# Optimization experiments

Measured on AMD Instinct MI355X. Metric: run time of the kernel, lower is better.

## Reference

```python
import jax, jax.numpy as jnp
import numpy as np

RANGE_DISP = 32
IND_INPUT_VIEW = np.array([1, 9]) - 1  # 0-based indices of the two input views
TOTAL_VIEWS = 9                         # an_sparse + an_novel
FEAT_CH = 64


def conv2d(x, w, b):
    # x: (N, Cin, H, W), w: (Cout, Cin, kh, kw), SAME padding, stride 1
    y = jax.lax.conv_general_dilated(x, w, (1, 1), 'SAME',
                                     dimension_numbers=('NCHW', 'OIHW', 'NCHW'))
    return y + b[None, :, None, None]


def unfold_1xK(x, K):
    # torch.nn.functional.unfold(x, kernel_size=(1, K)) for x: (M, C, H, W)
    # -> (M, C, K, H*(W-K+1)), column index = h*(W-K+1) + w (row-major).
    M, C, H, W = x.shape
    out_w = W - K + 1
    cols = jnp.arange(out_w)[None, :] + jnp.arange(K)[:, None]  # (K, out_w)
    y = x[:, :, :, cols]             # (M, C, H, K, out_w)
    y = y.transpose(0, 1, 3, 2, 4)   # (M, C, K, H, out_w)
    return y.reshape(M, C, K, H * out_w)


def setup_inputs() -> dict:
    key = jax.random.key(0)
    ks = jax.random.split(key, 24)
    b, an_sparse, an_novel, rp = 2, 2, 7, 32
    K = RANGE_DISP
    ps = rp + K - 1  # 63

    def rn(k, shape, s=1.0):
        return jax.random.normal(k, shape, dtype=jnp.float32) * s

    W = 0.05  # weight init scale
    return {
        'lf_sparse':        rn(ks[0], (b, an_sparse, rp, ps)),
        'flow_sparse':      rn(ks[1], (b, an_sparse, rp, ps)),
        'warped_lf_sparse': rn(ks[2], (b, an_sparse, rp, ps)),
        'patch_left':       rn(ks[3], (b, an_novel, rp, rp)),
        'patch_right':      rn(ks[4], (b, an_novel, rp, rp)),
        # FlowRefNet: 3 -> 64 -> 64 -> 64, 3x3 convs, SAME
        'fr_w1': rn(ks[5], (FEAT_CH, 3, 3, 3), W), 'fr_b1': jnp.zeros((FEAT_CH,), jnp.float32),
        'fr_w2': rn(ks[6], (FEAT_CH, FEAT_CH, 3, 3), W), 'fr_b2': jnp.zeros((FEAT_CH,), jnp.float32),
        'fr_w3': rn(ks[7], (FEAT_CH, FEAT_CH, 3, 3), W), 'fr_b3': jnp.zeros((FEAT_CH,), jnp.float32),
        # MlpNet: per-disparity MLP 67 -> 64 -> 64 -> 1 (weight head) + conf head 64 -> 1
        'mlp_w1': rn(ks[8], (67, 64), W), 'mlp_b1': jnp.zeros((64,), jnp.float32),
        'mlp_w2': rn(ks[9], (64, 64), W), 'mlp_b2': jnp.zeros((64,), jnp.float32),
        'mlp_w3': rn(ks[10], (64, 1), W), 'mlp_b3': jnp.zeros((1,), jnp.float32),
        'conf_w': rn(ks[11], (64, 1), W), 'conf_b': jnp.zeros((1,), jnp.float32),
        # ViewRefNet: 3 -> 64 -> 64 -> 1 convs, residual on novel patch
        'vr_w1': rn(ks[12], (FEAT_CH, 3, 3, 3), W), 'vr_b1': jnp.zeros((FEAT_CH,), jnp.float32),
        'vr_w2': rn(ks[13], (FEAT_CH, FEAT_CH, 3, 3), W), 'vr_b2': jnp.zeros((FEAT_CH,), jnp.float32),
        'vr_w3': rn(ks[14], (1, FEAT_CH, 3, 3), W), 'vr_b3': jnp.zeros((1,), jnp.float32),
    }


def reference(lf_sparse, flow_sparse, warped_lf_sparse, patch_left, patch_right,
              fr_w1, fr_b1, fr_w2, fr_b2, fr_w3, fr_b3,
              mlp_w1, mlp_b1, mlp_w2, mlp_b2, mlp_w3, mlp_b3, conf_w, conf_b,
              vr_w1, vr_b1, vr_w2, vr_b2, vr_w3, vr_b3):
    b, an_sparse, rp, ps = lf_sparse.shape
    an_novel = patch_left.shape[1]
    K = RANGE_DISP
    N = rp * rp

    lf = lf_sparse.reshape(b * an_sparse, 1, rp, ps)
    fl = flow_sparse.reshape(b * an_sparse, 1, rp, ps)
    wp = warped_lf_sparse.reshape(b * an_sparse, 1, rp, ps)

    # FlowRefNet: flow-feature extraction
    h = jax.nn.relu(conv2d(jnp.concatenate([fl, lf, wp], axis=1), fr_w1, fr_b1))
    h = jax.nn.relu(conv2d(h, fr_w2, fr_b2))
    feat = jax.nn.relu(conv2d(h, fr_w3, fr_b3))  # (b*as, 64, rp, ps)

    # angular code: input-view index minus novel-view index
    ind_novel = np.delete(np.arange(TOTAL_VIEWS), IND_INPUT_VIEW)
    ang = jnp.asarray(IND_INPUT_VIEW[None, :] - ind_novel[:, None], dtype=lf.dtype)  # (an, as)
    spatial = (jnp.arange(K) - K // 2).astype(lf.dtype)  # (K,)

    # EPI windows via unfold(kernel=(1, K))
    flow_unf = unfold_1xK(fl, K)[:, 0]  # (b*as, K, N)
    feat_unf = unfold_1xK(feat, K)      # (b*as, 64, K, N)

    sh = (b, an_novel, an_sparse)
    f_flow = jnp.broadcast_to(flow_unf.reshape(b, 1, an_sparse, 1, K, N),  sh + (1, K, N))
    f_feat = jnp.broadcast_to(feat_unf.reshape(b, 1, an_sparse, FEAT_CH, K, N), sh + (FEAT_CH, K, N))
    f_spat = jnp.broadcast_to(spatial.reshape(1, 1, 1, 1, K, 1),           sh + (1, K, N))
    f_ang  = jnp.broadcast_to(ang.reshape(1, an_novel, an_sparse, 1, 1, 1), sh + (1, K, N))
    features = jnp.concatenate([f_flow, f_feat, f_spat, f_ang], axis=3)  # (b, an, as, 67, K, N)
    # -> (b*an*as*N, K, 67) matching permute(0,3,2,1).reshape in torch
    features = features.transpose(0, 1, 2, 5, 4, 3).reshape(-1, K, 67)

    # MlpNet: per-disparity weight + per-sample confidence
    h1 = jax.nn.relu(features @ mlp_w1 + mlp_b1)
    h2 = jax.nn.relu(h1 @ mlp_w2 + mlp_b2)          # (M2, K, 64)
    weight = (h2 @ mlp_w3 + mlp_b3)[..., 0]         # (M2, K)
    conf = (h2.mean(axis=1) @ conf_w + conf_b)[..., 0]  # (M2,)

    weight = jax.nn.softmax(weight.reshape(b, an_novel, an_sparse, N, K), axis=-1)
    confs = jax.nn.softmax(conf.reshape(b, an_novel, an_sparse, N), axis=2)

    # disparity-weighted combination over EPI windows
    epi = unfold_1xK(lf, K)[:, 0].reshape(b, an_sparse, K, N)
    nv = jnp.einsum('bskn,bvsnk->bvsn', epi, weight)   # (b, an, as, N)
    novel = (nv * confs).sum(axis=2)                   # (b, an, N)

    # ViewRefNet: residual refinement
    pn = novel.reshape(b * an_novel, 1, rp, rp)
    pl = patch_left.reshape(b * an_novel, 1, rp, rp)
    pr = patch_right.reshape(b * an_novel, 1, rp, rp)
    g = jax.nn.relu(conv2d(jnp.concatenate([pn, pl, pr], axis=1), vr_w1, vr_b1))
    g = jax.nn.relu(conv2d(g, vr_w2, vr_b2))
    res = conv2d(g, vr_w3, vr_b3)
    out = pn + res
    return out.reshape(b, an_novel, rp, rp)
```

## Files before the change

kernel.cpp:

```cpp
#include <hip/hip_runtime.h>

typedef unsigned short u16;
typedef unsigned int u32;
typedef __bf16 bf16x8 __attribute__((ext_vector_type(8)));
typedef float f32x4 __attribute__((ext_vector_type(4)));
typedef u16 u16x8 __attribute__((ext_vector_type(8)));

__device__ __forceinline__ u16 f2bf(float f) {
    __bf16 h = (__bf16)f;
    return __builtin_bit_cast(u16, h);
}
__device__ __forceinline__ float bf2f(u16 u) {
    unsigned int x = ((unsigned int)u) << 16;
    return __builtin_bit_cast(float, x);
}

union FragU { u16x8 u; bf16x8 v; };

constexpr size_t WB2F  = 0;
constexpr size_t WB3F  = 18432;
constexpr size_t WBV2  = 36864;
constexpr size_t W1T   = 55296;
constexpr size_t W2T   = 57344;
constexpr size_t X1    = 59392;
constexpr size_t X2    = 317440;
constexpr size_t FEATBF= 575488;
constexpr size_t NVOFF = 833536;
constexpr size_t CFOFF = 862208;
constexpr size_t NOVEL = 890880;
constexpr size_t Y1    = 905216;
constexpr size_t Y2    = 1363968;

__global__ __launch_bounds__(256) void conv1feat_kernel(
    const float* __restrict__ in0, const float* __restrict__ in1,
    const float* __restrict__ in2,
    const float* __restrict__ wts, const float* __restrict__ bias,
    u16* __restrict__ out,
    const float* __restrict__ frw2, const float* __restrict__ frw3,
    const float* __restrict__ vrw2,
    const float* __restrict__ mw1, const float* __restrict__ mw2,
    u16* __restrict__ wb2, u16* __restrict__ wb3, u16* __restrict__ wbv,
    u16* __restrict__ w1t, u16* __restrict__ w2t)
{
    constexpr int W = 63, NPX = 2016, H = 32;
    const int t = threadIdx.x;
    if (blockIdx.z == 4) {
        const int tid = (blockIdx.y * 8 + blockIdx.x) * 256 + t;
        for (int i = tid; i < 36864; i += 16384) {
            int tap = i >> 12, och = (i >> 6) & 63, cin = i & 63;
            size_t s = (size_t)och * 576 + cin * 9 + tap;
            wb2[i] = f2bf(frw2[s]);
            wb3[i] = f2bf(frw3[s]);
            wbv[i] = f2bf(vrw2[s]);
        }
        for (int i = tid; i < 4096; i += 16384) {
            int col = i >> 6, r = i & 63;
            w1t[i] = f2bf(mw1[(1 + r) * 64 + col]);
            w2t[i] = f2bf(mw2[r * 64 + col]);
        }
        return;
    }
    const int px = blockIdx.y * 256 + t;
    const int m = blockIdx.z;
    const int og = blockIdx.x;
    if (px >= NPX) return;
    const int y = px / W, x = px - y * W;

    float acc[8];
#pragma unroll
    for (int oc = 0; oc < 8; ++oc) acc[oc] = bias[og * 8 + oc];

#pragma unroll
    for (int cin = 0; cin < 3; ++cin) {
        const float* ip = (cin == 0 ? in0 : (cin == 1 ? in1 : in2)) + (size_t)m * NPX;
        float tap[9];
#pragma unroll
        for (int dy = 0; dy < 3; ++dy) {
            int yy = y + dy - 1;
            bool ry = (yy >= 0) && (yy < H);
#pragma unroll
            for (int dx = 0; dx < 3; ++dx) {
                int xx = x + dx - 1;
                tap[dy * 3 + dx] = (ry && xx >= 0 && xx < W) ? ip[yy * W + xx] : 0.f;
            }
        }
#pragma unroll
        for (int oc = 0; oc < 8; ++oc) {
            const float* wr = wts + (size_t)(og * 8 + oc) * 27 + cin * 9;
#pragma unroll
            for (int j = 0; j < 9; ++j) acc[oc] = fmaf(tap[j], wr[j], acc[oc]);
        }
    }
    u16x8 pk;
#pragma unroll
    for (int oc = 0; oc < 8; ++oc) pk[oc] = f2bf(fmaxf(acc[oc], 0.f));
    *(u16x8*)(out + ((size_t)m * NPX + px) * 64 + og * 8) = pk;
}

template<int W, int NPX>
__global__ __launch_bounds__(256) void convmfma_kernel(
    const u16* __restrict__ in, const u16* __restrict__ wbf,
    const float* __restrict__ bias, u16* __restrict__ out)
{
    constexpr int H = 32;
    const int t = threadIdx.x;
    const int base = blockIdx.x * 64;
    const int ochb = blockIdx.y * 32;
    const int m = blockIdx.z;
    const int w = t >> 6, lane = t & 63, q = lane >> 4, l15 = lane & 15;

    const u16* im = in + (size_t)m * NPX * 64;
    const int pxA = base + w * 16 + l15;
    const int yA = pxA / W, xA = pxA - yA * W;
    const bool pxok = (pxA < NPX);

    f32x4 acc[2];
#pragma unroll
    for (int nt = 0; nt < 2; ++nt) acc[nt] = f32x4{0.f, 0.f, 0.f, 0.f};

#pragma unroll
    for (int tap = 0; tap < 9; ++tap) {
        const int dy = tap / 3 - 1, dx = tap % 3 - 1;
        const bool valid = pxok && (yA + dy >= 0) && (yA + dy < H)
                                && (xA + dx >= 0) && (xA + dx < W);
        const u16* ap = im + (size_t)(pxA + dy * W + dx) * 64;
        FragU a0, a1;
        if (valid) {
            a0 = *(const FragU*)(ap + q * 8);
            a1 = *(const FragU*)(ap + 32 + q * 8);
        } else {
#pragma unroll
            for (int jj = 0; jj < 8; ++jj) { a0.u[jj] = 0; a1.u[jj] = 0; }
        }
#pragma unroll
        for (int nt = 0; nt < 2; ++nt) {
            const u16* bp = wbf + tap * 4096 + (ochb + nt * 16 + l15) * 64;
            FragU b0 = *(const FragU*)(bp + q * 8);
            FragU b1 = *(const FragU*)(bp + 32 + q * 8);
            acc[nt] = __builtin_amdgcn_mfma_f32_16x16x32_bf16(a0.v, b0.v, acc[nt], 0, 0, 0);
            acc[nt] = __builtin_amdgcn_mfma_f32_16x16x32_bf16(a1.v, b1.v, acc[nt], 0, 0, 0);
        }
    }

#pragma unroll
    for (int nt = 0; nt < 2; ++nt) {
        const float bb = bias[ochb + nt * 16 + l15];
#pragma unroll
        for (int e = 0; e < 4; ++e) {
            int pxs = base + w * 16 + q * 4 + e;
            if (pxs < NPX)
                out[((size_t)m * NPX + pxs) * 64 + ochb + nt * 16 + l15] =
                    f2bf(fmaxf(acc[nt][e] + bb, 0.f));
        }
    }
}

__global__ __launch_bounds__(256, 2) void mlp_mfma_kernel(
    const float* __restrict__ lf, const float* __restrict__ flow,
    const u16* __restrict__ feat,
    const u16* __restrict__ w1t, const u16* __restrict__ w2t,
    const float* __restrict__ w1, const float* __restrict__ b1,
    const float* __restrict__ b2,
    const float* __restrict__ w3, const float* __restrict__ b3g,
    const float* __restrict__ cw, const float* __restrict__ cbg,
    float* __restrict__ nv_out, float* __restrict__ cf_out)
{
    constexpr int SBS = 72;
    __shared__ __align__(16) float s_vec[7 * 64];
    __shared__ __align__(16) float s_flow[256];
    __shared__ __align__(16) float s_epi[256];
    __shared__ __align__(16) u16 s_base[256 * SBS];

    const int t = threadIdx.x;
    const int blk = blockIdx.x;
    const int bs = blk >> 7;
    const int n0 = (blk & 127) * 8;
    const int b = bs >> 1, s = bs & 1;
    const int w = t >> 6, lane = t & 63, q = lane >> 4, l15 = lane & 15;

    if (t < 64) {
        s_vec[t]       = b1[t];
        s_vec[64 + t]  = b2[t];
        s_vec[128 + t] = w3[t];
        s_vec[192 + t] = cw[t];
        s_vec[256 + t] = w1[t];
        s_vec[320 + t] = w1[65 * 64 + t];
        s_vec[384 + t] = w1[66 * 64 + t];
    }
    {
        int nl = t >> 5, k = t & 31;
        int n = n0 + nl;
        int a = (bs * 32 + (n >> 5)) * 63 + (n & 31) + k;
        s_flow[t] = flow[a];
        s_epi[t]  = lf[a];
    }
    __syncthreads();

    const float b3s = b3g[0];
    const float cbs = cbg[0];

    FragU w1b[2][4];
#pragma unroll
    for (int ks = 0; ks < 2; ++ks)
#pragma unroll
        for (int nt = 0; nt < 4; ++nt)
            w1b[ks][nt] = *(const FragU*)(w1t + (nt * 16 + l15) * 64 + ks * 32 + q * 8);

    float w1r0pl[4], w1r65pl[4], b1pl[4];
#pragma unroll
    for (int nt = 0; nt < 4; ++nt) {
        int j1 = nt * 16 + l15;
        w1r0pl[nt]  = s_vec[256 + j1];
        w1r65pl[nt] = s_vec[320 + j1];
        b1pl[nt]    = s_vec[j1];
    }

#pragma unroll
    for (int mt = 0; mt < 4; ++mt) {
        const int rbase = w * 64 + mt * 16;
        FragU af[2];
        {
            int r = rbase + l15;
            int n = n0 + (r >> 5);
            int pos = (n >> 5) * 63 + (n & 31) + (r & 31);
            const u16* fp = feat + ((size_t)bs * 2016 + pos) * 64;
            af[0] = *(const FragU*)(fp + q * 8);
            af[1] = *(const FragU*)(fp + 32 + q * 8);
        }
// ... 29 lines not shown
        for (int jj = 0; jj < 8; ++jj)
            w66pl[ks][jj] = s_vec[384 + ks * 32 + q * 8 + jj];

    float b2pl[4][4], w3pl[4][4], cwpl[4][4];
#pragma unroll
    for (int mt = 0; mt < 4; ++mt)
#pragma unroll
        for (int e = 0; e < 4; ++e) {
            b2pl[mt][e] = s_vec[64 + mt * 16 + q * 4 + e];
            w3pl[mt][e] = s_vec[128 + mt * 16 + q * 4 + e];
            cwpl[mt][e] = s_vec[192 + mt * 16 + q * 4 + e];
        }
    float epi_pl[4];
#pragma unroll
    for (int nt = 0; nt < 4; ++nt) epi_pl[nt] = s_epi[w * 64 + nt * 16 + l15];

    for (int v = 0; v < 7; ++v) {
        float ang = (s == 0) ? -(float)(v + 1) : (float)(7 - v);
        f32x4 acc[4][4];
#pragma unroll
        for (int nt = 0; nt < 4; ++nt) {
            FragU bfr[2];
#pragma unroll
            for (int ks = 0; ks < 2; ++ks) {
                const u16x8 raw = *(const u16x8*)(s_base + (w * 64 + nt * 16 + l15) * SBS + ks * 32 + q * 8);
#pragma unroll
                for (int jj = 0; jj < 8; ++jj) {
                    float xv = bf2f(raw[jj]);
                    float hv = fmaxf(xv + ang * w66pl[ks][jj], 0.f);
                    bfr[ks].u[jj] = f2bf(hv);
                }
            }
#pragma unroll
            for (int mt = 0; mt < 4; ++mt) {
                f32x4 d = {0.f, 0.f, 0.f, 0.f};
                d = __builtin_amdgcn_mfma_f32_16x16x32_bf16(w2a[mt][0].v, bfr[0].v, d, 0, 0, 0);
                d = __builtin_amdgcn_mfma_f32_16x16x32_bf16(w2a[mt][1].v, bfr[1].v, d, 0, 0, 0);
                acc[mt][nt] = d;
            }
        }
        float wl[4], cfl[4];
#pragma unroll
        for (int nt = 0; nt < 4; ++nt) {
            float wls = 0.f, cfs = 0.f;
#pragma unroll
            for (int mt = 0; mt < 4; ++mt)
#pragma unroll
                for (int e = 0; e < 4; ++e) {
                    float h2 = fmaxf(acc[mt][nt][e] + b2pl[mt][e], 0.f);
                    wls += h2 * w3pl[mt][e];
                    cfs += h2 * cwpl[mt][e];
                }
            wls += __shfl_xor(wls, 16); wls += __shfl_xor(wls, 32);
            cfs += __shfl_xor(cfs, 16); cfs += __shfl_xor(cfs, 32);
            wl[nt]  = wls + b3s;
            cfl[nt] = cfs;
        }
#pragma unroll
        for (int ni = 0; ni < 2; ++ni) {
            float a0 = wl[ni * 2], a1 = wl[ni * 2 + 1];
            float mx = fmaxf(a0, a1);
#pragma unroll
            for (int msk = 1; msk <= 8; msk <<= 1) mx = fmaxf(mx, __shfl_xor(mx, msk));
            float e0 = __expf(a0 - mx), e1 = __expf(a1 - mx);
            float ssum = e0 + e1;
            float nvp = e0 * epi_pl[ni * 2] + e1 * epi_pl[ni * 2 + 1];
            float cfp = cfl[ni * 2] + cfl[ni * 2 + 1];
#pragma unroll
            for (int msk = 1; msk <= 8; msk <<= 1) {
                ssum += __shfl_xor(ssum, msk);
                nvp  += __shfl_xor(nvp, msk);
                cfp  += __shfl_xor(cfp, msk);
            }
            if (lane == 0) {
                int n = n0 + w * 2 + ni;
                size_t idx = ((size_t)(b * 7 + v) * 2 + s) * 1024 + n;
                nv_out[idx] = nvp / ssum;
                cf_out[idx] = cfp * (1.f / 32.f) + cbs;
            }
        }
    }
}

__global__ __launch_bounds__(256) void refconv1_kernel(
    const float* __restrict__ nv, const float* __restrict__ cf,
    const float* __restrict__ pl, const float* __restrict__ pr,
    const float* __restrict__ wts, const float* __restrict__ bias,
    u16* __restrict__ out, float* __restrict__ novel)
{
    __shared__ float pn[10][32];
    const int t = threadIdx.x;
    const int og = blockIdx.x, pt = blockIdx.y, m = blockIdx.z;
    const int y0 = pt * 8;

    for (int i = t; i < 320; i += 256) {
        int ri = i >> 5, col = i & 31;
        int gy = y0 - 1 + ri;
        float vv = 0.f;
        if (gy >= 0 && gy < 32) {
            int n = gy * 32 + col;
            size_t i0 = ((size_t)m * 2) * 1024 + n;
            size_t i1 = i0 + 1024;
            float c0 = cf[i0], c1 = cf[i1];
            float mx = fmaxf(c0, c1);
            float e0 = __expf(c0 - mx), e1 = __expf(c1 - mx);
            vv = (e0 * nv[i0] + e1 * nv[i1]) / (e0 + e1);
        }
        pn[ri][col] = vv;
    }
    __syncthreads();

    const int px = y0 * 32 + t;
    const int y = px >> 5, x = px & 31;
    if (og == 0) novel[(size_t)m * 1024 + px] = pn[y - y0 + 1][x];

    float acc[8];
#pragma unroll
    for (int oc = 0; oc < 8; ++oc) acc[oc] = bias[og * 8 + oc];

    {
        float tap[9];
#pragma unroll
        for (int dy = 0; dy < 3; ++dy) {
#pragma unroll
            for (int dx = 0; dx < 3; ++dx) {
                int gx = x + dx - 1;
                tap[dy * 3 + dx] = (gx >= 0 && gx < 32) ? pn[y - y0 + dy][gx] : 0.f;
            }
        }
#pragma unroll
        for (int oc = 0; oc < 8; ++oc) {
            const float* wr = wts + (size_t)(og * 8 + oc) * 27;
#pragma unroll
            for (int j = 0; j < 9; ++j) acc[oc] = fmaf(tap[j], wr[j], acc[oc]);
        }
    }
#pragma unroll
    for (int cin = 1; cin < 3; ++cin) {
        const float* ip = (cin == 1 ? pl : pr) + (size_t)m * 1024;
        float tap[9];
#pragma unroll
        for (int dy = 0; dy < 3; ++dy) {
            int yy = y + dy - 1;
            bool ry = (yy >= 0) && (yy < 32);
#pragma unroll
            for (int dx = 0; dx < 3; ++dx) {
                int xx = x + dx - 1;
                tap[dy * 3 + dx] = (ry && xx >= 0 && xx < 32) ? ip[yy * 32 + xx] : 0.f;
            }
        }
#pragma unroll
        for (int oc = 0; oc < 8; ++oc) {
            const float* wr = wts + (size_t)(og * 8 + oc) * 27 + cin * 9;
#pragma unroll
            for (int j = 0; j < 9; ++j) acc[oc] = fmaf(tap[j], wr[j], acc[oc]);
        }
    }
    u16x8 pk;
#pragma unroll
    for (int oc = 0; oc < 8; ++oc) pk[oc] = f2bf(fmaxf(acc[oc], 0.f));
    *(u16x8*)(out + ((size_t)m * 1024 + px) * 64 + og * 8) = pk;
}

__global__ __launch_bounds__(256) void convlast_kernel(
    const u16* __restrict__ in, const float* __restrict__ wts,
    const float* __restrict__ bias, const float* __restrict__ resid,
    float* __restrict__ out)
{
    __shared__ float sw3[576];
    const int t = threadIdx.x;
    for (int i = t; i < 576; i += 256) sw3[i] = wts[i];
    __syncthreads();

    const int tid = blockIdx.x * 256 + t;
    const int m = tid >> 10, p = tid & 1023;
    const int y = p >> 5, x = p & 31;
    float a = bias[0] + resid[tid];
    const u16* im = in + ((size_t)m * 1024 + p) * 64;
#pragma unroll
    for (int dy = 0; dy < 3; ++dy) {
        int yy = y + dy - 1;
        if (yy < 0 || yy >= 32) continue;
#pragma unroll
        for (int dx = 0; dx < 3; ++dx) {
            int xx = x + dx - 1;
            if (xx < 0 || xx >= 32) continue;
            const u16* ip = im + (size_t)((dy - 1) * 32 + (dx - 1)) * 64;
            const int tap = dy * 3 + dx;
#pragma unroll
            for (int cg = 0; cg < 8; ++cg) {
                u16x8 raw = *(const u16x8*)(ip + cg * 8);
#pragma unroll
                for (int e = 0; e < 8; ++e)
                    a = fmaf(bf2f(raw[e]), sw3[(cg * 8 + e) * 9 + tap], a);
            }
        }
    }
    out[tid] = a;
}

extern "C" void kernel_launch(void* const* d_in, const int* in_sizes, int n_in,
                              void* d_out, int out_size, void* d_ws, size_t ws_size,
                              hipStream_t stream) {
    const float* lf   = (const float*)d_in[0];
    const float* flow = (const float*)d_in[1];
    const float* wp   = (const float*)d_in[2];
    const float* pl   = (const float*)d_in[3];
    const float* pr   = (const float*)d_in[4];
    float* ws = (float*)d_ws;

    conv1feat_kernel<<<dim3(8, 8, 5), 256, 0, stream>>>(
        flow, lf, wp, (const float*)d_in[5], (const float*)d_in[6],
        (u16*)(ws + X1),
        (const float*)d_in[7], (const float*)d_in[9], (const float*)d_in[21],
        (const float*)d_in[11], (const float*)d_in[13],
        (u16*)(ws + WB2F), (u16*)(ws + WB3F), (u16*)(ws + WBV2),
        (u16*)(ws + W1T), (u16*)(ws + W2T));

    convmfma_kernel<63, 2016><<<dim3(32, 2, 4), 256, 0, stream>>>(
        (const u16*)(ws + X1), (const u16*)(ws + WB2F), (const float*)d_in[8],
        (u16*)(ws + X2));
    convmfma_kernel<63, 2016><<<dim3(32, 2, 4), 256, 0, stream>>>(
        (const u16*)(ws + X2), (const u16*)(ws + WB3F), (const float*)d_in[10],
        (u16*)(ws + FEATBF));

    mlp_mfma_kernel<<<512, 256, 0, stream>>>(
        lf, flow, (const u16*)(ws + FEATBF),
        (const u16*)(ws + W1T), (const u16*)(ws + W2T),
        (const float*)d_in[11], (const float*)d_in[12],
        (const float*)d_in[14],
        (const float*)d_in[15], (const float*)d_in[16],
        (const float*)d_in[17], (const float*)d_in[18],
        ws + NVOFF, ws + CFOFF);

    refconv1_kernel<<<dim3(8, 4, 14), 256, 0, stream>>>(
        ws + NVOFF, ws + CFOFF, pl, pr,
        (const float*)d_in[19], (const float*)d_in[20],
        (u16*)(ws + Y1), ws + NOVEL);
    convmfma_kernel<32, 1024><<<dim3(16, 2, 14), 256, 0, stream>>>(
        (const u16*)(ws + Y1), (const u16*)(ws + WBV2), (const float*)d_in[22],
        (u16*)(ws + Y2));
    convlast_kernel<<<56, 256, 0, stream>>>(
        (const u16*)(ws + Y2), (const float*)d_in[23], (const float*)d_in[24],
        ws + NOVEL, (float*)d_out);
}
```

Baseline: 184.3 us.

## Fuse the seven kernel launches into one cooperative persistent kernel with grid syncs

Replaces the sequence of seven separate kernel launches with a single cooperative kernel of 512 blocks that runs every stage in turn, separated by grid.sync barriers. Intermediate buffers still go through workspace memory. The goal is to remove per-launch overhead and the idle gaps between small kernels. In exchange, grid-wide barriers add sync cost, and later phases leave many blocks idle, since only 448 or 56 of them have work. The old multi-launch path is kept as a fallback if the cooperative launch fails.

```diff
diff --git a/kernel.cpp b/kernel.cpp
--- a/kernel.cpp
+++ b/kernel.cpp
@@ -1,4 +1,7 @@
 #include <hip/hip_runtime.h>
+#include <hip/hip_cooperative_groups.h>
+
+namespace cg = cooperative_groups;
 
 typedef unsigned short u16;
 typedef unsigned int u32;
@@ -30,6 +33,454 @@
 constexpr size_t NOVEL = 890880;
 constexpr size_t Y1    = 905216;
 constexpr size_t Y2    = 1363968;
+
+template<int W, int NPX, int LTILES, int LOCH, int NT>
+__device__ __forceinline__ void conv_mfma_phase(
+    int bid, int t, const u16* __restrict__ in, const u16* __restrict__ wbf,
+    const float* __restrict__ bias, u16* __restrict__ outp)
+{
+    constexpr int H = 32;
+    const int pxt  = bid % LTILES;
+    const int ochi = (bid / LTILES) % LOCH;
+    const int m    = bid / (LTILES * LOCH);
+    const int ochb = ochi * (NT * 16);
+    const int w = t >> 6, lane = t & 63, q = lane >> 4, l15 = lane & 15;
+    const int base = pxt * 64;
+    const u16* im = in + (size_t)m * NPX * 64;
+    const int pxA = base + w * 16 + l15;
+    const int yA = pxA / W, xA = pxA - yA * W;
+    const bool pxok = (pxA < NPX);
+
+    f32x4 acc[NT];
+#pragma unroll
+    for (int nt = 0; nt < NT; ++nt) acc[nt] = f32x4{0.f, 0.f, 0.f, 0.f};
+
+#pragma unroll
+    for (int tap = 0; tap < 9; ++tap) {
+        const int dy = tap / 3 - 1, dx = tap % 3 - 1;
+        const bool valid = pxok && (yA + dy >= 0) && (yA + dy < H)
+                                && (xA + dx >= 0) && (xA + dx < W);
+        const u16* ap = im + (size_t)(pxA + dy * W + dx) * 64;
+        FragU a0, a1;
+        if (valid) {
+            a0 = *(const FragU*)(ap + q * 8);
+            a1 = *(const FragU*)(ap + 32 + q * 8);
+        } else {
+#pragma unroll
+            for (int jj = 0; jj < 8; ++jj) { a0.u[jj] = 0; a1.u[jj] = 0; }
+        }
+#pragma unroll
+        for (int nt = 0; nt < NT; ++nt) {
+            const u16* bp = wbf + tap * 4096 + (ochb + nt * 16 + l15) * 64;
+            FragU b0 = *(const FragU*)(bp + q * 8);
+            FragU b1 = *(const FragU*)(bp + 32 + q * 8);
+            acc[nt] = __builtin_amdgcn_mfma_f32_16x16x32_bf16(a0.v, b0.v, acc[nt], 0, 0, 0);
+            acc[nt] = __builtin_amdgcn_mfma_f32_16x16x32_bf16(a1.v, b1.v, acc[nt], 0, 0, 0);
+        }
+    }
+
+#pragma unroll
+    for (int nt = 0; nt < NT; ++nt) {
+        const float bb = bias[ochb + nt * 16 + l15];
+#pragma unroll
+        for (int e = 0; e < 4; ++e) {
+            int pxs = base + w * 16 + q * 4 + e;
+            if (pxs < NPX)
+                outp[((size_t)m * NPX + pxs) * 64 + ochb + nt * 16 + l15] =
+                    f2bf(fmaxf(acc[nt][e] + bb, 0.f));
+        }
+    }
+}
+
+__global__ __launch_bounds__(256, 2) void fused_kernel(
+    const float* __restrict__ lf,   const float* __restrict__ flow,
+    const float* __restrict__ wp,   const float* __restrict__ pl,
+    const float* __restrict__ pr,
+    const float* __restrict__ frw1, const float* __restrict__ frb1,
+    const float* __restrict__ frw2, const float* __restrict__ frb2,
+    const float* __restrict__ frw3, const float* __restrict__ frb3,
+    const float* __restrict__ mw1,  const float* __restrict__ mb1,
+    const float* __restrict__ mw2,  const float* __restrict__ mb2,
+    const float* __restrict__ mw3,  const float* __restrict__ mb3,
+    const float* __restrict__ cw,   const float* __restrict__ cb,
+    const float* __restrict__ vrw1, const float* __restrict__ vrb1,
+    const float* __restrict__ vrw2, const float* __restrict__ vrb2,
+    const float* __restrict__ vrw3, const float* __restrict__ vrb3,
+    float* ws, float* __restrict__ out)
+{
+    __shared__ __align__(16) unsigned char smem[40704];
+
+    const int t = threadIdx.x;
+    const int bid = blockIdx.x;
+    cg::grid_group grid = cg::this_grid();
+
+    if (bid < 256) {
+        constexpr int W = 63, NPX = 2016, H = 32;
+        const int og = bid & 7;
+        const int m  = bid >> 6;
+        const int px = ((bid >> 3) & 7) * 256 + t;
+        if (px < NPX) {
+            const int y = px / W, x = px - y * W;
+            float acc[8];
+#pragma unroll
+            for (int oc = 0; oc < 8; ++oc) acc[oc] = frb1[og * 8 + oc];
+#pragma unroll
+            for (int cin = 0; cin < 3; ++cin) {
+                const float* ip = (cin == 0 ? flow : (cin == 1 ? lf : wp)) + (size_t)m * NPX;
+                float tap[9];
+#pragma unroll
+                for (int dy = 0; dy < 3; ++dy) {
+                    int yy = y + dy - 1;
+                    bool ry = (yy >= 0) && (yy < H);
+#pragma unroll
+                    for (int dx = 0; dx < 3; ++dx) {
+                        int xx = x + dx - 1;
+                        tap[dy * 3 + dx] = (ry && xx >= 0 && xx < W) ? ip[yy * W + xx] : 0.f;
+                    }
+                }
+#pragma unroll
+                for (int oc = 0; oc < 8; ++oc) {
+                    const float* wr = frw1 + (size_t)(og * 8 + oc) * 27 + cin * 9;
+#pragma unroll
+                    for (int j = 0; j < 9; ++j) acc[oc] = fmaf(tap[j], wr[j], acc[oc]);
+                }
+            }
+            u16x8 pk;
+#pragma unroll
+            for (int oc = 0; oc < 8; ++oc) pk[oc] = f2bf(fmaxf(acc[oc], 0.f));
+            *(u16x8*)((u16*)(ws + X1) + ((size_t)m * NPX + px) * 64 + og * 8) = pk;
+        }
+    } else if (bid < 320) {
+        const int tid = (bid - 256) * 256 + t;
+        u16* wb2 = (u16*)(ws + WB2F);
+        u16* wb3 = (u16*)(ws + WB3F);
+        u16* wbv = (u16*)(ws + WBV2);
+        u16* w1tp = (u16*)(ws + W1T);
+        u16* w2tp = (u16*)(ws + W2T);
+        for (int i = tid; i < 36864; i += 16384) {
+            int tap = i >> 12, och = (i >> 6) & 63, cin = i & 63;
+            size_t sgl = (size_t)och * 576 + cin * 9 + tap;
+            wb2[i] = f2bf(frw2[sgl]);
+            wb3[i] = f2bf(frw3[sgl]);
+            wbv[i] = f2bf(vrw2[sgl]);
+        }
+        for (int i = tid; i < 4096; i += 16384) {
+            int col = i >> 6, r = i & 63;
+            w1tp[i] = f2bf(mw1[(1 + r) * 64 + col]);
+            w2tp[i] = f2bf(mw2[r * 64 + col]);
+        }
+    }
+    grid.sync();
+
+    conv_mfma_phase<63, 2016, 32, 4, 1>(bid, t,
+        (const u16*)(ws + X1), (const u16*)(ws + WB2F), frb2, (u16*)(ws + X2));
+    grid.sync();
+
+    conv_mfma_phase<63, 2016, 32, 4, 1>(bid, t,
+        (const u16*)(ws + X2), (const u16*)(ws + WB3F), frb3, (u16*)(ws + FEATBF));
+    grid.sync();
+
+    {
+        constexpr int SBS = 72;
+        float* s_vec  = (float*)smem;
+        float* s_flow = (float*)(smem + 1792);
+        float* s_epi  = (float*)(smem + 2816);
+        u16*   s_base = (u16*)(smem + 3840);
+
+        const u16* feat = (const u16*)(ws + FEATBF);
+        const u16* w1t  = (const u16*)(ws + W1T);
+        const u16* w2t  = (const u16*)(ws + W2T);
+        float* nv_out = ws + NVOFF;
+        float* cf_out = ws + CFOFF;
+
+        const int blk = bid;
+        const int bs = blk >> 7;
+        const int n0 = (blk & 127) * 8;
+        const int b = bs >> 1, s = bs & 1;
+        const int w = t >> 6, lane = t & 63, q = lane >> 4, l15 = lane & 15;
+        (void)b;
+
+        if (t < 64) {
+            s_vec[t]       = mb1[t];
+            s_vec[64 + t]  = mb2[t];
+            s_vec[128 + t] = mw3[t];
+            s_vec[192 + t] = cw[t];
+            s_vec[256 + t] = mw1[t];
+            s_vec[320 + t] = mw1[65 * 64 + t];
+            s_vec[384 + t] = mw1[66 * 64 + t];
+        }
+        {
+            int nl = t >> 5, k = t & 31;
+            int n = n0 + nl;
+            int a = (bs * 32 + (n >> 5)) * 63 + (n & 31) + k;
+            s_flow[t] = flow[a];
+            s_epi[t]  = lf[a];
+        }
+        __syncthreads();
+
+        const float b3s = mb3[0];
+        const float cbs = cb[0];
+
+        FragU w1b[2][4];
+#pragma unroll
+        for (int ks = 0; ks < 2; ++ks)
+#pragma unroll
+            for (int nt = 0; nt < 4; ++nt)
+                w1b[ks][nt] = *(const FragU*)(w1t + (nt * 16 + l15) * 64 + ks * 32 + q * 8);
+
+        float w1r0pl[4], w1r65pl[4], b1pl[4];
+#pragma unroll
+        for (int nt = 0; nt < 4; ++nt) {
+            int j1 = nt * 16 + l15;
+            w1r0pl[nt]  = s_vec[256 + j1];
+            w1r65pl[nt] = s_vec[320 + j1];
+            b1pl[nt]    = s_vec[j1];
+        }
+
+#pragma unroll
+        for (int mt = 0; mt < 4; ++mt) {
+            const int rbase = w * 64 + mt * 16;
+            FragU af[2];
+            {
+                int r = rbase + l15;
+                int n = n0 + (r >> 5);
+                int pos = (n >> 5) * 63 + (n & 31) + (r & 31);
+                const u16* fp = feat + ((size_t)bs * 2016 + pos) * 64;
+                af[0] = *(const FragU*)(fp + q * 8);
+                af[1] = *(const FragU*)(fp + 32 + q * 8);
+            }
+            f32x4 flow4 = *(const f32x4*)(s_flow + rbase + q * 4);
+#pragma unroll
+            for (int nt = 0; nt < 4; ++nt) {
+                f32x4 d = {0.f, 0.f, 0.f, 0.f};
+                d = __builtin_amdgcn_mfma_f32_16x16x32_bf16(af[0].v, w1b[0][nt].v, d, 0, 0, 0);
+                d = __builtin_amdgcn_mfma_f32_16x16x32_bf16(af[1].v, w1b[1][nt].v, d, 0, 0, 0);
+#pragma unroll
+                for (int e = 0; e < 4; ++e) {
+                    int r = rbase + q * 4 + e;
+                    int k = r & 31;
+                    float val = d[e] + flow4[e] * w1r0pl[nt]
+                              + (float)(k - 16) * w1r65pl[nt] + b1pl[nt];
+                    s_base[r * SBS + nt * 16 + l15] = f2bf(val);
+                }
+            }
+        }
+        __syncthreads();
+
+        FragU w2a[4][2];
+#pragma unroll
+        for (int mt = 0; mt < 4; ++mt)
+#pragma unroll
+            for (int ks = 0; ks < 2; ++ks)
+                w2a[mt][ks] = *(const FragU*)(w2t + (mt * 16 + l15) * 64 + ks * 32 + q * 8);
+
+        float w66pl[2][8];
+#pragma unroll
+        for (int ks = 0; ks < 2; ++ks)
+#pragma unroll
+            for (int jj = 0; jj < 8; ++jj)
+                w66pl[ks][jj] = s_vec[384 + ks * 32 + q * 8 + jj];
+
+        float b2pl[4][4], w3pl[4][4], cwpl[4][4];
+#pragma unroll
+        for (int mt = 0; mt < 4; ++mt)
+#pragma unroll
+            for (int e = 0; e < 4; ++e) {
+                b2pl[mt][e] = s_vec[64 + mt * 16 + q * 4 + e];
+                w3pl[mt][e] = s_vec[128 + mt * 16 + q * 4 + e];
+                cwpl[mt][e] = s_vec[192 + mt * 16 + q * 4 + e];
+            }
+        float epi_pl[4];
+#pragma unroll
+        for (int nt = 0; nt < 4; ++nt) epi_pl[nt] = s_epi[w * 64 + nt * 16 + l15];
+
+        for (int v = 0; v < 7; ++v) {
+            float ang = (s == 0) ? -(float)(v + 1) : (float)(7 - v);
+            f32x4 acc[4][4];
+#pragma unroll
+            for (int nt = 0; nt < 4; ++nt) {
+                FragU bfr[2];
+#pragma unroll
+                for (int ks = 0; ks < 2; ++ks) {
+                    const u16x8 raw = *(const u16x8*)(s_base + (w * 64 + nt * 16 + l15) * SBS + ks * 32 + q * 8);
+#pragma unroll
+                    for (int jj = 0; jj < 8; ++jj) {
+                        float xv = bf2f(raw[jj]);
+                        float hv = fmaxf(xv + ang * w66pl[ks][jj], 0.f);
+                        bfr[ks].u[jj] = f2bf(hv);
+                    }
+                }
+#pragma unroll
+                for (int mt = 0; mt < 4; ++mt) {
+                    f32x4 d = {0.f, 0.f, 0.f, 0.f};
+                    d = __builtin_amdgcn_mfma_f32_16x16x32_bf16(w2a[mt][0].v, bfr[0].v, d, 0, 0, 0);
+                    d = __builtin_amdgcn_mfma_f32_16x16x32_bf16(w2a[mt][1].v, bfr[1].v, d, 0, 0, 0);
+                    acc[mt][nt] = d;
+                }
+            }
+            float wl[4], cfl[4];
+#pragma unroll
+            for (int nt = 0; nt < 4; ++nt) {
+                float wls = 0.f, cfs = 0.f;
+#pragma unroll
+                for (int mt = 0; mt < 4; ++mt)
+#pragma unroll
+                    for (int e = 0; e < 4; ++e) {
+                        float h2 = fmaxf(acc[mt][nt][e] + b2pl[mt][e], 0.f);
+                        wls += h2 * w3pl[mt][e];
+                        cfs += h2 * cwpl[mt][e];
+                    }
+                wls += __shfl_xor(wls, 16); wls += __shfl_xor(wls, 32);
+                cfs += __shfl_xor(cfs, 16); cfs += __shfl_xor(cfs, 32);
+                wl[nt]  = wls + b3s;
+                cfl[nt] = cfs;
+            }
+#pragma unroll
+            for (int ni = 0; ni < 2; ++ni) {
+                float a0 = wl[ni * 2], a1 = wl[ni * 2 + 1];
+                float mx = fmaxf(a0, a1);
+#pragma unroll
+                for (int msk = 1; msk <= 8; msk <<= 1) mx = fmaxf(mx, __shfl_xor(mx, msk));
+                float e0 = __expf(a0 - mx), e1 = __expf(a1 - mx);
+                float ssum = e0 + e1;
+                float nvp = e0 * epi_pl[ni * 2] + e1 * epi_pl[ni * 2 + 1];
+                float cfp = cfl[ni * 2] + cfl[ni * 2 + 1];
+#pragma unroll
+                for (int msk = 1; msk <= 8; msk <<= 1) {
+                    ssum += __shfl_xor(ssum, msk);
+                    nvp  += __shfl_xor(nvp, msk);
+                    cfp  += __shfl_xor(cfp, msk);
+                }
+                if (lane == 0) {
+                    int n = n0 + w * 2 + ni;
+                    size_t idx = ((size_t)((bs >> 1) * 7 + v) * 2 + s) * 1024 + n;
+                    nv_out[idx] = nvp / ssum;
+                    cf_out[idx] = cfp * (1.f / 32.f) + cbs;
+                }
+            }
+        }
+    }
+    grid.sync();
+
+    if (bid < 448) {
+        float (*pn)[32] = (float (*)[32])smem;
+        const float* nv = ws + NVOFF;
+        const float* cf = ws + CFOFF;
+        u16* outy1 = (u16*)(ws + Y1);
+        float* novel = ws + NOVEL;
+
+        const int og = bid & 7, pt = (bid >> 3) & 3, m = bid >> 5;
+        const int y0 = pt * 8;
+
+        for (int i = t; i < 320; i += 256) {
+            int ri = i >> 5, col = i & 31;
+            int gy = y0 - 1 + ri;
+            float vv = 0.f;
+            if (gy >= 0 && gy < 32) {
+                int n = gy * 32 + col;
+                size_t i0 = ((size_t)m * 2) * 1024 + n;
+                size_t i1 = i0 + 1024;
+                float c0 = cf[i0], c1 = cf[i1];
+                float mx = fmaxf(c0, c1);
+                float e0 = __expf(c0 - mx), e1 = __expf(c1 - mx);
+                vv = (e0 * nv[i0] + e1 * nv[i1]) / (e0 + e1);
+            }
+            pn[ri][col] = vv;
+        }
+        __syncthreads();
+
+        const int px = y0 * 32 + t;
+        const int y = px >> 5, x = px & 31;
+        if (og == 0) novel[(size_t)m * 1024 + px] = pn[y - y0 + 1][x];
+
+        float acc[8];
+#pragma unroll
+        for (int oc = 0; oc < 8; ++oc) acc[oc] = vrb1[og * 8 + oc];
+
+        {
+            float tap[9];
+#pragma unroll
+            for (int dy = 0; dy < 3; ++dy) {
+#pragma unroll
+                for (int dx = 0; dx < 3; ++dx) {
+                    int gx = x + dx - 1;
+                    tap[dy * 3 + dx] = (gx >= 0 && gx < 32) ? pn[y - y0 + dy][gx] : 0.f;
+                }
+            }
+#pragma unroll
+            for (int oc = 0; oc < 8; ++oc) {
+                const float* wr = vrw1 + (size_t)(og * 8 + oc) * 27;
+#pragma unroll
+                for (int j = 0; j < 9; ++j) acc[oc] = fmaf(tap[j], wr[j], acc[oc]);
+            }
+        }
+#pragma unroll
+        for (int cin = 1; cin < 3; ++cin) {
+            const float* ip = (cin == 1 ? pl : pr) + (size_t)m * 1024;
+            float tap[9];
+#pragma unroll
+            for (int dy = 0; dy < 3; ++dy) {
+                int yy = y + dy - 1;
+                bool ry = (yy >= 0) && (yy < 32);
+#pragma unroll
+                for (int dx = 0; dx < 3; ++dx) {
+                    int xx = x + dx - 1;
+                    tap[dy * 3 + dx] = (ry && xx >= 0 && xx < 32) ? ip[yy * 32 + xx] : 0.f;
+                }
+            }
+#pragma unroll
+            for (int oc = 0; oc < 8; ++oc) {
+                const float* wr = vrw1 + (size_t)(og * 8 + oc) * 27 + cin * 9;
+#pragma unroll
+                for (int j = 0; j < 9; ++j) acc[oc] = fmaf(tap[j], wr[j], acc[oc]);
+            }
+        }
+        u16x8 pk;
+#pragma unroll
+        for (int oc = 0; oc < 8; ++oc) pk[oc] = f2bf(fmaxf(acc[oc], 0.f));
+        *(u16x8*)(outy1 + ((size_t)m * 1024 + px) * 64 + og * 8) = pk;
+    }
+    grid.sync();
+
+    if (bid < 448)
+        conv_mfma_phase<32, 1024, 16, 2, 2>(bid, t,
+            (const u16*)(ws + Y1), (const u16*)(ws + WBV2), vrb2, (u16*)(ws + Y2));
+    grid.sync();
+
+    if (bid < 56) {
+        float* sw3 = (float*)smem;
+        const u16* in3 = (const u16*)(ws + Y2);
+        const float* resid = ws + NOVEL;
+        for (int i = t; i < 576; i += 256) sw3[i] = vrw3[i];
+        __syncthreads();
+
+        const int tid = bid * 256 + t;
+        const int m = tid >> 10, p = tid & 1023;
+        const int y = p >> 5, x = p & 31;
+        float a = vrb3[0] + resid[tid];
+        const u16* im = in3 + ((size_t)m * 1024 + p) * 64;
+#pragma unroll
+        for (int dy = 0; dy < 3; ++dy) {
+            int yy = y + dy - 1;
+            if (yy < 0 || yy >= 32) continue;
+#pragma unroll
+            for (int dx = 0; dx < 3; ++dx) {
+                int xx = x + dx - 1;
+                if (xx < 0 || xx >= 32) continue;
+                const u16* ip = im + (size_t)((dy - 1) * 32 + (dx - 1)) * 64;
+                const int tap = dy * 3 + dx;
+#pragma unroll
+                for (int cg2 = 0; cg2 < 8; ++cg2) {
+                    u16x8 raw = *(const u16x8*)(ip + cg2 * 8);
+#pragma unroll
+                    for (int e = 0; e < 8; ++e)
+                        a = fmaf(bf2f(raw[e]), sw3[(cg2 * 8 + e) * 9 + tap], a);
+                }
+            }
+        }
+        out[tid] = a;
+    }
+}
 
 __global__ __launch_bounds__(256) void conv1feat_kernel(
     const float* __restrict__ in0, const float* __restrict__ in1,
@@ -445,11 +896,11 @@
             const u16* ip = im + (size_t)((dy - 1) * 32 + (dx - 1)) * 64;
             const int tap = dy * 3 + dx;
 #pragma unroll
-            for (int cg = 0; cg < 8; ++cg) {
-                u16x8 raw = *(const u16x8*)(ip + cg * 8);
+            for (int cg2 = 0; cg2 < 8; ++cg2) {
+                u16x8 raw = *(const u16x8*)(ip + cg2 * 8);
 #pragma unroll
                 for (int e = 0; e < 8; ++e)
-                    a = fmaf(bf2f(raw[e]), sw3[(cg * 8 + e) * 9 + tap], a);
+                    a = fmaf(bf2f(raw[e]), sw3[(cg2 * 8 + e) * 9 + tap], a);
             }
         }
     }
@@ -464,40 +915,70 @@
     const float* wp   = (const float*)d_in[2];
     const float* pl   = (const float*)d_in[3];
     const float* pr   = (const float*)d_in[4];
+    const float* frw1 = (const float*)d_in[5];
+    const float* frb1 = (const float*)d_in[6];
+    const float* frw2 = (const float*)d_in[7];
+    const float* frb2 = (const float*)d_in[8];
+    const float* frw3 = (const float*)d_in[9];
+    const float* frb3 = (const float*)d_in[10];
+    const float* mw1  = (const float*)d_in[11];
+    const float* mb1  = (const float*)d_in[12];
+    const float* mw2  = (const float*)d_in[13];
+    const float* mb2  = (const float*)d_in[14];
+    const float* mw3  = (const float*)d_in[15];
+    const float* mb3  = (const float*)d_in[16];
+    const float* cw   = (const float*)d_in[17];
+    const float* cb   = (const float*)d_in[18];
+    const float* vrw1 = (const float*)d_in[19];
+    const float* vrb1 = (const float*)d_in[20];
+    const float* vrw2 = (const float*)d_in[21];
+    const float* vrb2 = (const float*)d_in[22];
+    const float* vrw3 = (const float*)d_in[23];
+    const float* vrb3 = (const float*)d_in[24];
     float* ws = (float*)d_ws;
-
-    conv1feat_kernel<<<dim3(8, 8, 5), 256, 0, stream>>>(
-        flow, lf, wp, (const float*)d_in[5], (const float*)d_in[6],
-        (u16*)(ws + X1),
-        (const float*)d_in[7], (const float*)d_in[9], (const float*)d_in[21],
-        (const float*)d_in[11], (const float*)d_in[13],
-        (u16*)(ws + WB2F), (u16*)(ws + WB3F), (u16*)(ws + WBV2),
-        (u16*)(ws + W1T), (u16*)(ws + W2T));
-
-    convmfma_kernel<63, 2016><<<dim3(32, 2, 4), 256, 0, stream>>>(
-        (const u16*)(ws + X1), (const u16*)(ws + WB2F), (const float*)d_in[8],
-        (u16*)(ws + X2));
-    convmfma_kernel<63, 2016><<<dim3(32, 2, 4), 256, 0, stream>>>(
-        (const u16*)(ws + X2), (const u16*)(ws + WB3F), (const float*)d_in[10],
-        (u16*)(ws + FEATBF));
-
-    mlp_mfma_kernel<<<512, 256, 0, stream>>>(
-        lf, flow, (const u16*)(ws + FEATBF),
-        (const u16*)(ws + W1T), (const u16*)(ws + W2T),
-        (const float*)d_in[11], (const float*)d_in[12],
-        (const float*)d_in[14],
-        (const float*)d_in[15], (const float*)d_in[16],
-        (const float*)d_in[17], (const float*)d_in[18],
-        ws + NVOFF, ws + CFOFF);
-
-    refconv1_kernel<<<dim3(8, 4, 14), 256, 0, stream>>>(
-        ws + NVOFF, ws + CFOFF, pl, pr,
-        (const float*)d_in[19], (const float*)d_in[20],
-        (u16*)(ws + Y1), ws + NOVEL);
-    convmfma_kernel<32, 1024><<<dim3(16, 2, 14), 256, 0, stream>>>(
-        (const u16*)(ws + Y1), (const u16*)(ws + WBV2), (const float*)d_in[22],
-        (u16*)(ws + Y2));
-    convlast_kernel<<<56, 256, 0, stream>>>(
-        (const u16*)(ws + Y2), (const float*)d_in[23], (const float*)d_in[24],
-        ws + NOVEL, (float*)d_out);
+    float* outp = (float*)d_out;
+
+    void* params[] = {
+        &lf, &flow, &wp, &pl, &pr,
+        &frw1, &frb1, &frw2, &frb2, &frw3, &frb3,
+        &mw1, &mb1, &mw2, &mb2, &mw3, &mb3,
+        &cw, &cb,
+        &vrw1, &vrb1, &vrw2, &vrb2, &vrw3, &vrb3,
+        &ws, &outp
+    };
+
+    hipError_t err = hipLaunchCooperativeKernel(
+        (const void*)fused_kernel, dim3(512), dim3(256), params, 0u, stream);
+
+    if (err != hipSuccess) {
+        conv1feat_kernel<<<dim3(8, 8, 5), 256, 0, stream>>>(
+            flow, lf, wp, frw1, frb1,
+            (u16*)(ws + X1),
+            frw2, frw3, vrw2, mw1, mw2,
+            (u16*)(ws + WB2F), (u16*)(ws + WB3F), (u16*)(ws + WBV2),
+            (u16*)(ws + W1T), (u16*)(ws + W2T));
+
+        convmfma_kernel<63, 2016><<<dim3(32, 2, 4), 256, 0, stream>>>(
+            (const u16*)(ws + X1), (const u16*)(ws + WB2F), frb2,
+            (u16*)(ws + X2));
+        convmfma_kernel<63, 2016><<<dim3(32, 2, 4), 256, 0, stream>>>(
+            (const u16*)(ws + X2), (const u16*)(ws + WB3F), frb3,
+            (u16*)(ws + FEATBF));
+
+        mlp_mfma_kernel<<<512, 256, 0, stream>>>(
+            lf, flow, (const u16*)(ws + FEATBF),
+            (const u16*)(ws + W1T), (const u16*)(ws + W2T),
+            mw1, mb1, mb2, mw3, mb3, cw, cb,
+            ws + NVOFF, ws + CFOFF);
+
+        refconv1_kernel<<<dim3(8, 4, 14), 256, 0, stream>>>(
+            ws + NVOFF, ws + CFOFF, pl, pr, vrw1, vrb1,
+            (u16*)(ws + Y1), ws + NOVEL);
+        convmfma_kernel<32, 1024><<<dim3(16, 2, 14), 256, 0, stream>>>(
+            (const u16*)(ws + Y1), (const u16*)(ws + WBV2), vrb2,
+            (u16*)(ws + Y2));
+        convlast_kernel<<<56, 256, 0, stream>>>(
+            (const u16*)(ws + Y2), vrw3, vrb3,
+            ws + NOVEL, (float*)d_out);
+    }
 }
```

Result: slower. 543.8 us (+195.0%).

## Fuse ViewRefNet convs into one LDS-tiled kernel and split feature convs finer

Applied to the files above, without the earlier changes.

Merges the three ViewRefNet stages (novel-view combine plus conv1, the MFMA conv2, and the final 64-to-1 conv with residual) into a single kernel. Each block handles a 4-row tile and keeps the halo-extended intermediates in swizzled shared memory. This removes two launches and the global round trips for the Y1, Y2 and NOVEL buffers, at the cost of recomputing halo rows and running only 112 blocks. Separately, the FlowRefNet MFMA convs now use 16 output channels per block instead of 32, which doubles the grid to give more parallelism.

```diff
diff --git a/kernel.cpp b/kernel.cpp
--- a/kernel.cpp
+++ b/kernel.cpp
@@ -27,9 +27,6 @@
 constexpr size_t FEATBF= 575488;
 constexpr size_t NVOFF = 833536;
 constexpr size_t CFOFF = 862208;
-constexpr size_t NOVEL = 890880;
-constexpr size_t Y1    = 905216;
-constexpr size_t Y2    = 1363968;
 
 __global__ __launch_bounds__(256) void conv1feat_kernel(
     const float* __restrict__ in0, const float* __restrict__ in1,
@@ -97,7 +94,7 @@
     *(u16x8*)(out + ((size_t)m * NPX + px) * 64 + og * 8) = pk;
 }
 
-template<int W, int NPX>
+template<int W, int NPX, int NT>
 __global__ __launch_bounds__(256) void convmfma_kernel(
     const u16* __restrict__ in, const u16* __restrict__ wbf,
     const float* __restrict__ bias, u16* __restrict__ out)
@@ -105,7 +102,7 @@
     constexpr int H = 32;
     const int t = threadIdx.x;
     const int base = blockIdx.x * 64;
-    const int ochb = blockIdx.y * 32;
+    const int ochb = blockIdx.y * (NT * 16);
     const int m = blockIdx.z;
     const int w = t >> 6, lane = t & 63, q = lane >> 4, l15 = lane & 15;
 
@@ -114,9 +111,9 @@
     const int yA = pxA / W, xA = pxA - yA * W;
     const bool pxok = (pxA < NPX);
 
-    f32x4 acc[2];
-#pragma unroll
-    for (int nt = 0; nt < 2; ++nt) acc[nt] = f32x4{0.f, 0.f, 0.f, 0.f};
+    f32x4 acc[NT];
+#pragma unroll
+    for (int nt = 0; nt < NT; ++nt) acc[nt] = f32x4{0.f, 0.f, 0.f, 0.f};
 
 #pragma unroll
     for (int tap = 0; tap < 9; ++tap) {
@@ -133,7 +130,7 @@
             for (int jj = 0; jj < 8; ++jj) { a0.u[jj] = 0; a1.u[jj] = 0; }
         }
 #pragma unroll
-        for (int nt = 0; nt < 2; ++nt) {
+        for (int nt = 0; nt < NT; ++nt) {
             const u16* bp = wbf + tap * 4096 + (ochb + nt * 16 + l15) * 64;
             FragU b0 = *(const FragU*)(bp + q * 8);
             FragU b1 = *(const FragU*)(bp + 32 + q * 8);
@@ -143,7 +140,7 @@
     }
 
 #pragma unroll
-    for (int nt = 0; nt < 2; ++nt) {
+    for (int nt = 0; nt < NT; ++nt) {
         const float bb = bias[ochb + nt * 16 + l15];
 #pragma unroll
         for (int e = 0; e < 4; ++e) {
@@ -339,20 +336,27 @@
     }
 }
 
-__global__ __launch_bounds__(256) void refconv1_kernel(
+__global__ __launch_bounds__(512) void refine_kernel(
     const float* __restrict__ nv, const float* __restrict__ cf,
     const float* __restrict__ pl, const float* __restrict__ pr,
-    const float* __restrict__ wts, const float* __restrict__ bias,
-    u16* __restrict__ out, float* __restrict__ novel)
+    const float* __restrict__ vrw1, const float* __restrict__ vrb1,
+    const u16* __restrict__ wbv, const float* __restrict__ vrb2,
+    const float* __restrict__ vrw3, const float* __restrict__ vrb3,
+    float* __restrict__ out)
 {
-    __shared__ float pn[10][32];
+    __shared__ __align__(16) float pn_s[10][32];
+    __shared__ __align__(16) float sw3[576];
+    __shared__ __align__(16) u16 g1_s[8 * 32 * 64];
+    __shared__ __align__(16) u16 g2_s[6 * 32 * 64];
+
     const int t = threadIdx.x;
-    const int og = blockIdx.x, pt = blockIdx.y, m = blockIdx.z;
-    const int y0 = pt * 8;
-
-    for (int i = t; i < 320; i += 256) {
-        int ri = i >> 5, col = i & 31;
-        int gy = y0 - 1 + ri;
+    const int pt = blockIdx.x;
+    const int m  = blockIdx.y;
+    const int y0 = pt * 4;
+
+    if (t < 320) {
+        int rr = t >> 5, col = t & 31;
+        int gy = y0 - 3 + rr;
         float vv = 0.f;
         if (gy >= 0 && gy < 32) {
             int n = gy * 32 + col;
@@ -363,97 +367,147 @@
             float e0 = __expf(c0 - mx), e1 = __expf(c1 - mx);
             vv = (e0 * nv[i0] + e1 * nv[i1]) / (e0 + e1);
         }
-        pn[ri][col] = vv;
-    }
+        pn_s[rr][col] = vv;
+    }
+    for (int i = t; i < 576; i += 512) sw3[i] = vrw3[i];
     __syncthreads();
 
-    const int px = y0 * 32 + t;
-    const int y = px >> 5, x = px & 31;
-    if (og == 0) novel[(size_t)m * 1024 + px] = pn[y - y0 + 1][x];
-
-    float acc[8];
-#pragma unroll
-    for (int oc = 0; oc < 8; ++oc) acc[oc] = bias[og * 8 + oc];
-
     {
-        float tap[9];
+        const int px_i = t >> 1;
+        const int oh   = t & 1;
+        const int lr0  = px_i >> 5;
+        const int x    = px_i & 31;
+        const int gy   = y0 - 2 + lr0;
+        const bool inimg = (gy >= 0) && (gy < 32);
+
+        float tap0[9], tap1[9], tap2[9];
+        if (inimg) {
+            const float* plm = pl + (size_t)m * 1024;
+            const float* prm = pr + (size_t)m * 1024;
+#pragma unroll
+            for (int dy = 0; dy < 3; ++dy) {
+                int prow = lr0 + dy;
+                int yy = gy + dy - 1;
+                bool ry = (yy >= 0) && (yy < 32);
+#pragma unroll
+                for (int dx = 0; dx < 3; ++dx) {
+                    int xx = x + dx - 1;
+                    bool rx = (xx >= 0) && (xx < 32);
+                    tap0[dy * 3 + dx] = rx ? pn_s[prow][xx] : 0.f;
+                    tap1[dy * 3 + dx] = (ry && rx) ? plm[yy * 32 + xx] : 0.f;
+                    tap2[dy * 3 + dx] = (ry && rx) ? prm[yy * 32 + xx] : 0.f;
+                }
+            }
+        }
+#pragma unroll
+        for (int jg = 0; jg < 4; ++jg) {
+            u16x8 pk;
+#pragma unroll
+            for (int e = 0; e < 8; ++e) {
+                float acc = 0.f;
+                if (inimg) {
+                    int o = oh * 32 + jg * 8 + e;
+                    const float* wr = vrw1 + (size_t)o * 27;
+                    acc = vrb1[o];
+#pragma unroll
+                    for (int j = 0; j < 9; ++j) acc = fmaf(tap0[j], wr[j], acc);
+#pragma unroll
+                    for (int j = 0; j < 9; ++j) acc = fmaf(tap1[j], wr[9 + j], acc);
+#pragma unroll
+                    for (int j = 0; j < 9; ++j) acc = fmaf(tap2[j], wr[18 + j], acc);
+                    acc = fmaxf(acc, 0.f);
+                }
+                pk[e] = f2bf(acc);
+            }
+            int byte = (px_i * 128 + oh * 64 + jg * 16) ^ ((px_i & 7) << 4);
+            *(u16x8*)((char*)g1_s + byte) = pk;
+        }
+    }
+    __syncthreads();
+
+    {
+        const int w = t >> 6, lane = t & 63, q = lane >> 4, l15 = lane & 15;
+        const int ocht = w & 3, base = ocht * 16;
+        const int wg = w >> 2;
+
+        f32x4 acc[6];
+#pragma unroll
+        for (int i = 0; i < 6; ++i) acc[i] = f32x4{0.f, 0.f, 0.f, 0.f};
+
+#pragma unroll
+        for (int tap = 0; tap < 9; ++tap) {
+            const int dy = tap / 3 - 1, dx = tap % 3 - 1;
+            const u16* bp = wbv + tap * 4096 + (base + l15) * 64;
+            FragU b0 = *(const FragU*)(bp + q * 8);
+            FragU b1 = *(const FragU*)(bp + 32 + q * 8);
+#pragma unroll
+            for (int i = 0; i < 6; ++i) {
+                const int p = (wg + 2 * i) * 16 + l15;
+                const int xx = (p & 31) + dx;
+                const int p1 = p + (dy + 1) * 32 + dx;
+                FragU a0, a1;
+                if (xx >= 0 && xx < 32) {
+                    int byte = (p1 * 128 + q * 16) ^ ((p1 & 7) << 4);
+                    a0 = *(const FragU*)((const char*)g1_s + byte);
+                    byte = (p1 * 128 + 64 + q * 16) ^ ((p1 & 7) << 4);
+                    a1 = *(const FragU*)((const char*)g1_s + byte);
+                } else {
+#pragma unroll
+                    for (int jj = 0; jj < 8; ++jj) { a0.u[jj] = 0; a1.u[jj] = 0; }
+                }
+                acc[i] = __builtin_amdgcn_mfma_f32_16x16x32_bf16(a0.v, b0.v, acc[i], 0, 0, 0);
+                acc[i] = __builtin_amdgcn_mfma_f32_16x16x32_bf16(a1.v, b1.v, acc[i], 0, 0, 0);
+            }
+        }
+
+        const float bb = vrb2[base + l15];
+#pragma unroll
+        for (int i = 0; i < 6; ++i) {
+#pragma unroll
+            for (int e = 0; e < 4; ++e) {
+                int p = (wg + 2 * i) * 16 + q * 4 + e;
+                int gy2 = y0 - 1 + (p >> 5);
+                float vv = (gy2 >= 0 && gy2 < 32) ? fmaxf(acc[i][e] + bb, 0.f) : 0.f;
+                int byte = (p * 128 + (base + l15) * 2) ^ ((p & 7) << 4);
+                *(u16*)((char*)g2_s + byte) = f2bf(vv);
+            }
+        }
+    }
+    __syncthreads();
+
+    {
+        const int px_i = t >> 2;
+        const int part = t & 3;
+        const int ly = px_i >> 5;
+        const int x  = px_i & 31;
+
+        float a = 0.f;
 #pragma unroll
         for (int dy = 0; dy < 3; ++dy) {
-#pragma unroll
-            for (int dx = 0; dx < 3; ++dx) {
-                int gx = x + dx - 1;
-                tap[dy * 3 + dx] = (gx >= 0 && gx < 32) ? pn[y - y0 + dy][gx] : 0.f;
-            }
-        }
-#pragma unroll
-        for (int oc = 0; oc < 8; ++oc) {
-            const float* wr = wts + (size_t)(og * 8 + oc) * 27;
-#pragma unroll
-            for (int j = 0; j < 9; ++j) acc[oc] = fmaf(tap[j], wr[j], acc[oc]);
-        }
-    }
-#pragma unroll
-    for (int cin = 1; cin < 3; ++cin) {
-        const float* ip = (cin == 1 ? pl : pr) + (size_t)m * 1024;
-        float tap[9];
-#pragma unroll
-        for (int dy = 0; dy < 3; ++dy) {
-            int yy = y + dy - 1;
-            bool ry = (yy >= 0) && (yy < 32);
 #pragma unroll
             for (int dx = 0; dx < 3; ++dx) {
                 int xx = x + dx - 1;
-                tap[dy * 3 + dx] = (ry && xx >= 0 && xx < 32) ? ip[yy * 32 + xx] : 0.f;
-            }
-        }
-#pragma unroll
-        for (int oc = 0; oc < 8; ++oc) {
-            const float* wr = wts + (size_t)(og * 8 + oc) * 27 + cin * 9;
-#pragma unroll
-            for (int j = 0; j < 9; ++j) acc[oc] = fmaf(tap[j], wr[j], acc[oc]);
-        }
-    }
-    u16x8 pk;
-#pragma unroll
-    for (int oc = 0; oc < 8; ++oc) pk[oc] = f2bf(fmaxf(acc[oc], 0.f));
-    *(u16x8*)(out + ((size_t)m * 1024 + px) * 64 + og * 8) = pk;
-}
-
-__global__ __launch_bounds__(256) void convlast_kernel(
-    const u16* __restrict__ in, const float* __restrict__ wts,
-    const float* __restrict__ bias, const float* __restrict__ resid,
-    float* __restrict__ out)
-{
-    __shared__ float sw3[576];
-    const int t = threadIdx.x;
-    for (int i = t; i < 576; i += 256) sw3[i] = wts[i];
-    __syncthreads();
-
-    const int tid = blockIdx.x * 256 + t;
-    const int m = tid >> 10, p = tid & 1023;
-    const int y = p >> 5, x = p & 31;
-    float a = bias[0] + resid[tid];
-    const u16* im = in + ((size_t)m * 1024 + p) * 64;
-#pragma unroll
-    for (int dy = 0; dy < 3; ++dy) {
-        int yy = y + dy - 1;
-        if (yy < 0 || yy >= 32) continue;
-#pragma unroll
-        for (int dx = 0; dx < 3; ++dx) {
-            int xx = x + dx - 1;
-            if (xx < 0 || xx >= 32) continue;
-            const u16* ip = im + (size_t)((dy - 1) * 32 + (dx - 1)) * 64;
-            const int tap = dy * 3 + dx;
-#pragma unroll
-            for (int cg = 0; cg < 8; ++cg) {
-                u16x8 raw = *(const u16x8*)(ip + cg * 8);
-#pragma unroll
-                for (int e = 0; e < 8; ++e)
-                    a = fmaf(bf2f(raw[e]), sw3[(cg * 8 + e) * 9 + tap], a);
-            }
-        }
-    }
-    out[tid] = a;
+                if (xx < 0 || xx >= 32) continue;
+                int p2 = px_i + dy * 32 + dx - 1;
+                const int tap = dy * 3 + dx;
+                int byte0 = (p2 * 128 + part * 32) ^ ((p2 & 7) << 4);
+                int byte1 = (p2 * 128 + part * 32 + 16) ^ ((p2 & 7) << 4);
+                u16x8 r0 = *(const u16x8*)((const char*)g2_s + byte0);
+                u16x8 r1 = *(const u16x8*)((const char*)g2_s + byte1);
+#pragma unroll
+                for (int e = 0; e < 8; ++e) {
+                    a = fmaf(bf2f(r0[e]), sw3[(part * 16 + e) * 9 + tap], a);
+                    a = fmaf(bf2f(r1[e]), sw3[(part * 16 + 8 + e) * 9 + tap], a);
+                }
+            }
+        }
+        a += __shfl_xor(a, 1);
+        a += __shfl_xor(a, 2);
+        if (part == 0) {
+            int gy = y0 + ly;
+            out[(size_t)m * 1024 + gy * 32 + x] = pn_s[ly + 3][x] + a + vrb3[0];
+        }
+    }
 }
 
 extern "C" void kernel_launch(void* const* d_in, const int* in_sizes, int n_in,
@@ -474,10 +528,10 @@
         (u16*)(ws + WB2F), (u16*)(ws + WB3F), (u16*)(ws + WBV2),
         (u16*)(ws + W1T), (u16*)(ws + W2T));
 
-    convmfma_kernel<63, 2016><<<dim3(32, 2, 4), 256, 0, stream>>>(
+    convmfma_kernel<63, 2016, 1><<<dim3(32, 4, 4), 256, 0, stream>>>(
         (const u16*)(ws + X1), (const u16*)(ws + WB2F), (const float*)d_in[8],
         (u16*)(ws + X2));
-    convmfma_kernel<63, 2016><<<dim3(32, 2, 4), 256, 0, stream>>>(
+    convmfma_kernel<63, 2016, 1><<<dim3(32, 4, 4), 256, 0, stream>>>(
         (const u16*)(ws + X2), (const u16*)(ws + WB3F), (const float*)d_in[10],
         (u16*)(ws + FEATBF));
 
@@ -490,14 +544,10 @@
         (const float*)d_in[17], (const float*)d_in[18],
         ws + NVOFF, ws + CFOFF);
 
-    refconv1_kernel<<<dim3(8, 4, 14), 256, 0, stream>>>(
+    refine_kernel<<<dim3(8, 14), 512, 0, stream>>>(
         ws + NVOFF, ws + CFOFF, pl, pr,
         (const float*)d_in[19], (const float*)d_in[20],
-        (u16*)(ws + Y1), ws + NOVEL);
-    convmfma_kernel<32, 1024><<<dim3(16, 2, 14), 256, 0, stream>>>(
-        (const u16*)(ws + Y1), (const u16*)(ws + WBV2), (const float*)d_in[22],
-        (u16*)(ws + Y2));
-    convlast_kernel<<<56, 256, 0, stream>>>(
-        (const u16*)(ws + Y2), (const float*)d_in[23], (const float*)d_in[24],
-        ws + NOVEL, (float*)d_out);
-}
+        (const u16*)(ws + WBV2), (const float*)d_in[22],
+        (const float*)d_in[23], (const float*)d_in[24],
+        (float*)d_out);
+}
```

Result: slower. 189.3 us (+2.7%).
